# Performance work log

Hardware: AMD Instinct MI355X
Metric: run time of the kernel (lower is better)

The kernel has to match this reference:

```python
import jax, jax.numpy as jnp
import numpy as np

B, T, E = 8, 2048, 512   # batch, tokens, embedding_dim
K, C = 8192, 8           # num_embeddings, codebook_dim
LN_EPS = 1e-5


def _layer_norm(x, g, b):
    mu = jnp.mean(x, axis=-1, keepdims=True)
    var = jnp.var(x, axis=-1, keepdims=True)
    return (x - mu) * jax.lax.rsqrt(var + LN_EPS) * g + b


def setup_inputs() -> dict:
    key = jax.random.key(0)
    ks = jax.random.split(key, 8)
    s_e = 1.0 / np.sqrt(E)
    s_c = 1.0 / np.sqrt(C)
    return {
        "features": jax.random.normal(ks[0], (B, T, E), dtype=jnp.float32),
        # project_in: Linear(E,E) -> ReLU -> Linear(E,C)
        "W1_in": jax.random.uniform(ks[1], (E, E), jnp.float32, -s_e, s_e),
        "b1_in": jnp.zeros((E,), jnp.float32),
        "W2_in": jax.random.uniform(ks[2], (E, C), jnp.float32, -s_e, s_e),
        "b2_in": jnp.zeros((C,), jnp.float32),
        "ln_in_g": jnp.ones((C,), jnp.float32),
        "ln_in_b": jnp.zeros((C,), jnp.float32),
        # codebook
        "emb": jax.random.normal(ks[3], (K, C), dtype=jnp.float32),
        # project_out: Linear(C,E) -> ReLU -> Linear(E,E)
        "W1_out": jax.random.uniform(ks[4], (C, E), jnp.float32, -s_c, s_c),
        "b1_out": jnp.zeros((E,), jnp.float32),
        "W2_out": jax.random.uniform(ks[5], (E, E), jnp.float32, -s_e, s_e),
        "b2_out": jnp.zeros((E,), jnp.float32),
        "ln_out_g": jnp.ones((E,), jnp.float32),
        "ln_out_b": jnp.zeros((E,), jnp.float32),
    }


def reference(features, W1_in, b1_in, W2_in, b2_in, ln_in_g, ln_in_b, emb,
              W1_out, b1_out, W2_out, b2_out, ln_out_g, ln_out_b):
    # project_in + norm_in
    h = jax.nn.relu(jnp.einsum('bte,ef->btf', features, W1_in) + b1_in)
    z = jnp.einsum('bte,ec->btc', h, W2_in) + b2_in          # (B,T,C)
    z = _layer_norm(z, ln_in_g, ln_in_b)
    zf = z.reshape(-1, C)                                     # (N,C)
    d = (jnp.sum(zf * zf, axis=1, keepdims=True)
         - 2.0 * zf @ emb.T
         + jnp.sum(emb * emb, axis=1)[None, :])               # (N,K)
    idx = jnp.argmin(d, axis=1)                               # (N,)
    encodings = jax.nn.one_hot(idx, K, dtype=zf.dtype)        # (N,K)
    quantized = emb[idx]                                      # gather == one_hot @ emb
    # project_out + norm_out
    q = jax.nn.relu(quantized @ W1_out + b1_out)
    q = q @ W2_out + b2_out
    q = _layer_norm(q, ln_out_g, ln_out_b)
    q = q.reshape(B, T, E)
    return q, idx[:, None], encodings
```

## Files before the change

### kernel.cpp

```cpp
#include <hip/hip_runtime.h>
#include <cstdint>
#include <cstddef>

#define N_TOK 16384
#define E_DIM 512
#define C_DIM 8
#define K_CODES 8192
#define LN_EPS 1e-5f

typedef __attribute__((ext_vector_type(8))) short short8;
typedef __attribute__((ext_vector_type(4))) float f32x4;

__device__ __forceinline__ unsigned short bf16_rn(float x) {
  unsigned u = __float_as_uint(x);
  unsigned r = u + 0x7FFFu + ((u >> 16) & 1u);
  return (unsigned short)(r >> 16);
}
__device__ __forceinline__ float bf16_f(unsigned short h) {
  return __uint_as_float(((unsigned)h) << 16);
}

__device__ __forceinline__ void gload16(const void* g, void* l) {
  __builtin_amdgcn_global_load_lds(
      (const __attribute__((address_space(1))) void*)g,
      (__attribute__((address_space(3))) void*)l, 16, 0, 0);
}

__global__ __launch_bounds__(256) void pack_a(const float* __restrict__ A,
    unsigned short* __restrict__ hi, unsigned short* __restrict__ lo) {
  int t = blockIdx.x * 256 + threadIdx.x;
  int l = t & 63;
  int kt = (t >> 6) & 15;
  int mf = t >> 10;
  const float* src = A + (size_t)(mf * 16 + (l & 15)) * 512 + kt * 32 + (l >> 4) * 8;
  float4 x0 = *(const float4*)src;
  float4 x1 = *(const float4*)(src + 4);
  float xs[8] = {x0.x, x0.y, x0.z, x0.w, x1.x, x1.y, x1.z, x1.w};
  unsigned hw[4], lw[4];
#pragma unroll
  for (int p = 0; p < 4; ++p) {
    float a = xs[2 * p], b = xs[2 * p + 1];
    unsigned short ha = bf16_rn(a), hb = bf16_rn(b);
    unsigned short la = bf16_rn(a - bf16_f(ha)), lb = bf16_rn(b - bf16_f(hb));
    hw[p] = (unsigned)ha | ((unsigned)hb << 16);
    lw[p] = (unsigned)la | ((unsigned)lb << 16);
  }
  uint4 hv; hv.x = hw[0]; hv.y = hw[1]; hv.z = hw[2]; hv.w = hw[3];
  uint4 lv; lv.x = lw[0]; lv.y = lw[1]; lv.z = lw[2]; lv.w = lw[3];
  ((uint4*)hi)[t] = hv;
  ((uint4*)lo)[t] = lv;
}

__global__ __launch_bounds__(256) void pack_b(const float* __restrict__ B,
    unsigned short* __restrict__ hi, unsigned short* __restrict__ lo) {
  int t = blockIdx.x * 256 + threadIdx.x;
  int l = t & 63;
  int kt = (t >> 6) & 15;
  int nf = t >> 10;
  int col = nf * 16 + (l & 15);
  int krow = kt * 32 + (l >> 4) * 8;
  unsigned hw[4], lw[4];
#pragma unroll
  for (int p = 0; p < 4; ++p) {
    float a = B[(size_t)(krow + 2 * p) * 512 + col];
    float b = B[(size_t)(krow + 2 * p + 1) * 512 + col];
    unsigned short ha = bf16_rn(a), hb = bf16_rn(b);
    unsigned short la = bf16_rn(a - bf16_f(ha)), lb = bf16_rn(b - bf16_f(hb));
    hw[p] = (unsigned)ha | ((unsigned)hb << 16);
    lw[p] = (unsigned)la | ((unsigned)lb << 16);
  }
  uint4 hv; hv.x = hw[0]; hv.y = hw[1]; hv.z = hw[2]; hv.w = hw[3];
  uint4 lv; lv.x = lw[0]; lv.y = lw[1]; lv.z = lw[2]; lv.w = lw[3];
  ((uint4*)hi)[t] = hv;
  ((uint4*)lo)[t] = lv;
}

template<bool RELU>
__global__ __launch_bounds__(256) void gemm_mfma(const unsigned short* __restrict__ Ah,
    const unsigned short* __restrict__ Al, const unsigned short* __restrict__ Bh,
    const unsigned short* __restrict__ Bl, const float* __restrict__ bias,
    float* __restrict__ C) {
  __shared__ char smem[32768];
  const int tid = threadIdx.x;
  const int l = tid & 63;
  const int w = tid >> 6;
  const int wm = w >> 1, wn = w & 1;
  const int mblk = blockIdx.y, nblk = blockIdx.x;

  char* sAh = smem;
  char* sAl = smem + 8192;
  char* sBh = smem + 16384;
  char* sBl = smem + 24576;

  const char* gAh = (const char*)Ah + (((size_t)(mblk * 8 + 2 * w) * 16) * 64 + l) * 16;
  const char* gAl = (const char*)Al + (((size_t)(mblk * 8 + 2 * w) * 16) * 64 + l) * 16;
  const char* gBh = (const char*)Bh + (((size_t)(nblk * 8 + 2 * w) * 16) * 64 + l) * 16;
  const char* gBl = (const char*)Bl + (((size_t)(nblk * 8 + 2 * w) * 16) * 64 + l) * 16;
  char* dA0 = sAh + (2 * w) * 1024;
  char* dA1 = sAl + (2 * w) * 1024;
  char* dB0 = sBh + (2 * w) * 1024;
  char* dB1 = sBl + (2 * w) * 1024;

  f32x4 acc[4][4];
#pragma unroll
  for (int i = 0; i < 4; ++i)
#pragma unroll
    for (int j = 0; j < 4; ++j) acc[i][j] = (f32x4){0.f, 0.f, 0.f, 0.f};

  for (int kt = 0; kt < 16; ++kt) {
    __syncthreads();
    const size_t ko = (size_t)kt * 1024;
    gload16(gAh + ko,           dA0);
    gload16(gAh + ko + 16384,   dA0 + 1024);
    gload16(gAl + ko,           dA1);
    gload16(gAl + ko + 16384,   dA1 + 1024);
    gload16(gBh + ko,           dB0);
    gload16(gBh + ko + 16384,   dB0 + 1024);
    gload16(gBl + ko,           dB1);
    gload16(gBl + ko + 16384,   dB1 + 1024);
    __syncthreads();

    short8 a_h[4], a_l[4], b_h[4], b_l[4];
#pragma unroll
    for (int i = 0; i < 4; ++i) {
      a_h[i] = ((const short8*)sAh)[(wm * 4 + i) * 64 + l];
      a_l[i] = ((const short8*)sAl)[(wm * 4 + i) * 64 + l];
    }
#pragma unroll
    for (int j = 0; j < 4; ++j) {
      b_h[j] = ((const short8*)sBh)[(wn * 4 + j) * 64 + l];
      b_l[j] = ((const short8*)sBl)[(wn * 4 + j) * 64 + l];
    }
#pragma unroll
    for (int i = 0; i < 4; ++i)
#pragma unroll
      for (int j = 0; j < 4; ++j) {
        acc[i][j] = __builtin_amdgcn_mfma_f32_16x16x32_bf16(a_h[i], b_h[j], acc[i][j], 0, 0, 0);
        acc[i][j] = __builtin_amdgcn_mfma_f32_16x16x32_bf16(a_h[i], b_l[j], acc[i][j], 0, 0, 0);
        acc[i][j] = __builtin_amdgcn_mfma_f32_16x16x32_bf16(a_l[i], b_h[j], acc[i][j], 0, 0, 0);
      }
  }

  const int colb = nblk * 128 + wn * 64 + (l & 15);
  const int rowb = mblk * 128 + wm * 64 + ((l >> 4) << 2);
#pragma unroll
  for (int j = 0; j < 4; ++j) {
    float bv = bias[colb + j * 16];
#pragma unroll
    for (int i = 0; i < 4; ++i) {
#pragma unroll
      for (int r = 0; r < 4; ++r) {
        float v = acc[i][j][r] + bv;
        if (RELU) v = fmaxf(v, 0.f);
        C[(size_t)(rowb + i * 16 + r) * 512 + colb + j * 16] = v;
      }
    }
  }
}

__global__ __launch_bounds__(256) void zln_kernel(const float* __restrict__ h,
    const float* __restrict__ W2, const float* __restrict__ b2,
    const float* __restrict__ g, const float* __restrict__ b,
    float* __restrict__ z) {
  int token = blockIdx.x * 4 + (threadIdx.x >> 6);
  int lane = threadIdx.x & 63;
  const float* hr = h + (size_t)token * E_DIM;
  float acc[C_DIM];
#pragma unroll
  for (int c = 0; c < C_DIM; ++c) acc[c] = 0.f;
  for (int e = lane; e < E_DIM; e += 64) {
    float hv = hr[e];
    const float* w = W2 + e * C_DIM;
#pragma unroll
    for (int c = 0; c < C_DIM; ++c) acc[c] = fmaf(hv, w[c], acc[c]);
  }
#pragma unroll
  for (int c = 0; c < C_DIM; ++c) {
#pragma unroll
    for (int off = 32; off > 0; off >>= 1) acc[c] += __shfl_down(acc[c], off);
  }
  if (lane == 0) {
    float v[C_DIM]; float mu = 0.f;
#pragma unroll
    for (int c = 0; c < C_DIM; ++c) { v[c] = acc[c] + b2[c]; mu += v[c]; }
    mu *= 0.125f;
    float var = 0.f;
#pragma unroll
    for (int c = 0; c < C_DIM; ++c) { float d = v[c] - mu; var += d * d; }
    var *= 0.125f;
    float inv = 1.0f / sqrtf(var + LN_EPS);
#pragma unroll
    for (int c = 0; c < C_DIM; ++c)
      z[(size_t)token * C_DIM + c] = ((v[c] - mu) * inv) * g[c] + b[c];
  }
}

__global__ void ne_kernel(const float* __restrict__ emb, float* __restrict__ ne) {
  int k = blockIdx.x * 256 + threadIdx.x;
  const float* e = emb + (size_t)k * C_DIM;
  float s = 0.f;
#pragma unroll
  for (int c = 0; c < C_DIM; ++c) s = fmaf(e[c], e[c], s);
  ne[k] = s;
}

__global__ __launch_bounds__(256) void vq_partial(const float* __restrict__ z,
    const float* __restrict__ emb, const float* __restrict__ ne,
    float* __restrict__ pbest, int* __restrict__ pidx) {
  int chunk = blockIdx.x & 7;
  int token = (blockIdx.x >> 3) * 256 + threadIdx.x;
  float zv[C_DIM];
#pragma unroll
  for (int c = 0; c < C_DIM; ++c) zv[c] = z[(size_t)token * C_DIM + c];
  float s = 0.f;
#pragma unroll
  for (int c = 0; c < C_DIM; ++c) s = fmaf(zv[c], zv[c], s);
  float best = 3.402823466e38f; int bi = 0;
  int j0 = chunk * 1024;
  for (int j = j0; j < j0 + 1024; ++j) {
    const float* e = emb + (size_t)j * C_DIM;
    float p = 0.f;
#pragma unroll
    for (int c = 0; c < C_DIM; ++c) p = fmaf(zv[c], e[c], p);
    float d = fmaf(-2.f, p, s) + ne[j];
    if (d < best) { best = d; bi = j; }
  }
  pbest[chunk * N_TOK + token] = best;
  pidx[chunk * N_TOK + token] = bi;
}

__global__ void vq_combine(const float* __restrict__ pbest, const int* __restrict__ pidx,
    int* __restrict__ idx_i, float* __restrict__ idxf) {
  int n = blockIdx.x * 256 + threadIdx.x;
  float best = pbest[n]; int bi = pidx[n];
#pragma unroll
  for (int c = 1; c < 8; ++c) {
    float bb = pbest[c * N_TOK + n]; int i2 = pidx[c * N_TOK + n];
    if (bb < best) { best = bb; bi = i2; }
  }
  idx_i[n] = bi;
  idxf[n] = (float)bi;
}

__global__ __launch_bounds__(128) void proj_out1(const float* __restrict__ emb,
    const float* __restrict__ W1, const float* __restrict__ b1, float* __restrict__ t) {
  int k = blockIdx.x;
  int e = threadIdx.x * 4;
  float4 acc = *(const float4*)(b1 + e);
#pragma unroll
  for (int c = 0; c < C_DIM; ++c) {
    float ev = emb[(size_t)k * C_DIM + c];
    float4 w = *(const float4*)(W1 + (size_t)c * E_DIM + e);
    acc.x = fmaf(ev, w.x, acc.x); acc.y = fmaf(ev, w.y, acc.y);
    acc.z = fmaf(ev, w.z, acc.z); acc.w = fmaf(ev, w.w, acc.w);
  }
  acc.x = fmaxf(acc.x, 0.f); acc.y = fmaxf(acc.y, 0.f);
  acc.z = fmaxf(acc.z, 0.f); acc.w = fmaxf(acc.w, 0.f);
  *(float4*)(t + (size_t)k * E_DIM + e) = acc;
}

__global__ __launch_bounds__(256) void ln512(float* __restrict__ g,
    const float* __restrict__ gw, const float* __restrict__ bw) {
  int row = blockIdx.x; int tid = threadIdx.x;
  float* r = g + (size_t)row * E_DIM;
  float v0 = r[tid], v1 = r[tid + 256];
  __shared__ float red[8];
  int lane = tid & 63, wid = tid >> 6;
  float sum = v0 + v1;
#pragma unroll
  for (int off = 32; off > 0; off >>= 1) sum += __shfl_xor(sum, off);
  if (lane == 0) red[wid] = sum;
  __syncthreads();
  float mu = (red[0] + red[1] + red[2] + red[3]) * (1.0f / 512.0f);
  float d0 = v0 - mu, d1 = v1 - mu;
  float sq = d0 * d0 + d1 * d1;
#pragma unroll
  for (int off = 32; off > 0; off >>= 1) sq += __shfl_xor(sq, off);
  if (lane == 0) red[4 + wid] = sq;
  __syncthreads();
  float var = (red[4] + red[5] + red[6] + red[7]) * (1.0f / 512.0f);
  float inv = 1.0f / sqrtf(var + LN_EPS);
  r[tid]       = (d0 * inv) * gw[tid] + bw[tid];
  r[tid + 256] = (d1 * inv) * gw[tid + 256] + bw[tid + 256];
}

__global__ __launch_bounds__(128) void out_gather(const float* __restrict__ oc,
    const int* __restrict__ idx_i, float* __restrict__ q) {
  int n = blockIdx.x;
  int k = idx_i[n];
  int e = threadIdx.x * 4;
  *(float4*)(q + (size_t)n * E_DIM + e) = *(const float4*)(oc + (size_t)k * E_DIM + e);
}

__global__ void scatter_ones(const float* __restrict__ idxf, float* __restrict__ enc) {
  int n = blockIdx.x * 256 + threadIdx.x;
  int k = (int)idxf[n];
  enc[(size_t)n * K_CODES + k] = 1.0f;
}

extern "C" void kernel_launch(void* const* d_in, const int* in_sizes, int n_in,
                              void* d_out, int out_size, void* d_ws, size_t ws_size,
                              hipStream_t stream) {
  const float* features = (const float*)d_in[0];
  const float* W1_in  = (const float*)d_in[1];
  const float* b1_in  = (const float*)d_in[2];
  const float* W2_in  = (const float*)d_in[3];
  const float* b2_in  = (const float*)d_in[4];
  const float* ln_in_g = (const float*)d_in[5];
  const float* ln_in_b = (const float*)d_in[6];
  const float* emb    = (const float*)d_in[7];
  const float* W1_out = (const float*)d_in[8];
  const float* b1_out = (const float*)d_in[9];
  const float* W2_out = (const float*)d_in[10];
  const float* b2_out = (const float*)d_in[11];
  const float* ln_out_g = (const float*)d_in[12];
  const float* ln_out_b = (const float*)d_in[13];

  float* q    = (float*)d_out;
  float* idxf = q + (size_t)N_TOK * E_DIM;
  float* enc  = idxf + N_TOK;

  float* h     = enc;
  float* t     = enc + 8388608;
  float* g     = enc + 12582912;
  float* z     = enc + 16777216;
  float* ne    = enc + 16908288;
  float* pbest = enc + 16916480;
  int*   idx_i = (int*)(enc + 17047552);
  int*   pidx  = (int*)(enc + 17063936);
  unsigned short* A1h = (unsigned short*)(enc + 17195008);
  unsigned short* A1l = (unsigned short*)(enc + 21389312);
  unsigned short* A2h = (unsigned short*)(enc + 25583616);
  unsigned short* A2l = (unsigned short*)(enc + 27680768);
  unsigned short* B1h = (unsigned short*)(enc + 29777920);
  unsigned short* B1l = (unsigned short*)(enc + 29908992);
  unsigned short* B2h = (unsigned short*)(enc + 30040064);
  unsigned short* B2l = (unsigned short*)(enc + 30171136);

  ne_kernel<<<K_CODES / 256, 256, 0, stream>>>(emb, ne);

  pack_b<<<128, 256, 0, stream>>>(W1_in, B1h, B1l);
  pack_a<<<4096, 256, 0, stream>>>(features, A1h, A1l);
  dim3 g1(4, N_TOK / 128);
  gemm_mfma<true><<<g1, 256, 0, stream>>>(A1h, A1l, B1h, B1l, b1_in, h);

  zln_kernel<<<N_TOK / 4, 256, 0, stream>>>(h, W2_in, b2_in, ln_in_g, ln_in_b, z);

  vq_partial<<<(N_TOK / 256) * 8, 256, 0, stream>>>(z, emb, ne, pbest, pidx);
  vq_combine<<<N_TOK / 256, 256, 0, stream>>>(pbest, pidx, idx_i, idxf);

  proj_out1<<<K_CODES, 128, 0, stream>>>(emb, W1_out, b1_out, t);
  pack_b<<<128, 256, 0, stream>>>(W2_out, B2h, B2l);
  pack_a<<<2048, 256, 0, stream>>>(t, A2h, A2l);
  dim3 g2(4, K_CODES / 128);
  gemm_mfma<false><<<g2, 256, 0, stream>>>(A2h, A2l, B2h, B2l, b2_out, g);

  ln512<<<K_CODES, 256, 0, stream>>>(g, ln_out_g, ln_out_b);

  out_gather<<<N_TOK, 128, 0, stream>>>(g, idx_i, q);

  hipMemsetAsync(enc, 0, (size_t)N_TOK * K_CODES * sizeof(float), stream);
  scatter_ones<<<N_TOK / 256, 256, 0, stream>>>(idxf, enc);
}
```

Measured before the change: 793.8 us.

## Fuse pack kernels into prep, double-buffer GEMM LDS, fuse proj_out1 with packing

Merges the ne, pack_a and both pack_b launches into a single prep kernel. It also fuses the first output projection with bf16 hi/lo packing, so the float intermediate t is never written or re-read. The MFMA GEMM now double-buffers LDS stages so the next k-tile's global-to-LDS loads are issued while the current tile computes. LDS use doubles to 64KB per block, which may lower occupancy.

```diff
diff --git a/kernel.cpp b/kernel.cpp
--- a/kernel.cpp
+++ b/kernel.cpp
@@ -26,9 +26,8 @@
       (__attribute__((address_space(3))) void*)l, 16, 0, 0);
 }
 
-__global__ __launch_bounds__(256) void pack_a(const float* __restrict__ A,
-    unsigned short* __restrict__ hi, unsigned short* __restrict__ lo) {
-  int t = blockIdx.x * 256 + threadIdx.x;
+__device__ __forceinline__ void pack_a_body(const float* __restrict__ A,
+    unsigned short* __restrict__ hi, unsigned short* __restrict__ lo, int t) {
   int l = t & 63;
   int kt = (t >> 6) & 15;
   int mf = t >> 10;
@@ -51,9 +50,8 @@
   ((uint4*)lo)[t] = lv;
 }
 
-__global__ __launch_bounds__(256) void pack_b(const float* __restrict__ B,
-    unsigned short* __restrict__ hi, unsigned short* __restrict__ lo) {
-  int t = blockIdx.x * 256 + threadIdx.x;
+__device__ __forceinline__ void pack_b_body(const float* __restrict__ B,
+    unsigned short* __restrict__ hi, unsigned short* __restrict__ lo, int t) {
   int l = t & 63;
   int kt = (t >> 6) & 15;
   int nf = t >> 10;
@@ -75,31 +73,47 @@
   ((uint4*)lo)[t] = lv;
 }
 
+__global__ __launch_bounds__(256) void prep(const float* __restrict__ features,
+    const float* __restrict__ W1_in, const float* __restrict__ W2_out,
+    const float* __restrict__ emb,
+    unsigned short* __restrict__ A1h, unsigned short* __restrict__ A1l,
+    unsigned short* __restrict__ B1h, unsigned short* __restrict__ B1l,
+    unsigned short* __restrict__ B2h, unsigned short* __restrict__ B2l,
+    float* __restrict__ ne) {
+  int bid = blockIdx.x;
+  int tid = threadIdx.x;
+  if (bid < 4096) {
+    pack_a_body(features, A1h, A1l, bid * 256 + tid);
+  } else if (bid < 4224) {
+    pack_b_body(W1_in, B1h, B1l, (bid - 4096) * 256 + tid);
+  } else if (bid < 4352) {
+    pack_b_body(W2_out, B2h, B2l, (bid - 4224) * 256 + tid);
+  } else {
+    int k = (bid - 4352) * 256 + tid;
+    const float* e = emb + (size_t)k * C_DIM;
+    float s = 0.f;
+#pragma unroll
+    for (int c = 0; c < C_DIM; ++c) s = fmaf(e[c], e[c], s);
+    ne[k] = s;
+  }
+}
+
 template<bool RELU>
 __global__ __launch_bounds__(256) void gemm_mfma(const unsigned short* __restrict__ Ah,
     const unsigned short* __restrict__ Al, const unsigned short* __restrict__ Bh,
     const unsigned short* __restrict__ Bl, const float* __restrict__ bias,
     float* __restrict__ C) {
-  __shared__ char smem[32768];
+  __shared__ char smem[65536];
   const int tid = threadIdx.x;
   const int l = tid & 63;
   const int w = tid >> 6;
   const int wm = w >> 1, wn = w & 1;
   const int mblk = blockIdx.y, nblk = blockIdx.x;
 
-  char* sAh = smem;
-  char* sAl = smem + 8192;
-  char* sBh = smem + 16384;
-  char* sBl = smem + 24576;
-
   const char* gAh = (const char*)Ah + (((size_t)(mblk * 8 + 2 * w) * 16) * 64 + l) * 16;
   const char* gAl = (const char*)Al + (((size_t)(mblk * 8 + 2 * w) * 16) * 64 + l) * 16;
   const char* gBh = (const char*)Bh + (((size_t)(nblk * 8 + 2 * w) * 16) * 64 + l) * 16;
   const char* gBl = (const char*)Bl + (((size_t)(nblk * 8 + 2 * w) * 16) * 64 + l) * 16;
-  char* dA0 = sAh + (2 * w) * 1024;
-  char* dA1 = sAl + (2 * w) * 1024;
-  char* dB0 = sBh + (2 * w) * 1024;
-  char* dB1 = sBl + (2 * w) * 1024;
 
   f32x4 acc[4][4];
 #pragma unroll
@@ -107,29 +121,39 @@
 #pragma unroll
     for (int j = 0; j < 4; ++j) acc[i][j] = (f32x4){0.f, 0.f, 0.f, 0.f};
 
-  for (int kt = 0; kt < 16; ++kt) {
-    __syncthreads();
+  auto stage = [&](int buf, int kt) {
+    char* base = smem + buf * 32768;
     const size_t ko = (size_t)kt * 1024;
-    gload16(gAh + ko,           dA0);
-    gload16(gAh + ko + 16384,   dA0 + 1024);
-    gload16(gAl + ko,           dA1);
-    gload16(gAl + ko + 16384,   dA1 + 1024);
-    gload16(gBh + ko,           dB0);
-    gload16(gBh + ko + 16384,   dB0 + 1024);
-    gload16(gBl + ko,           dB1);
-    gload16(gBl + ko + 16384,   dB1 + 1024);
-    __syncthreads();
-
+    char* dA0 = base + (2 * w) * 1024;
+    char* dA1 = base + 8192 + (2 * w) * 1024;
+    char* dB0 = base + 16384 + (2 * w) * 1024;
+    char* dB1 = base + 24576 + (2 * w) * 1024;
+    gload16(gAh + ko,         dA0);
+    gload16(gAh + ko + 16384, dA0 + 1024);
+    gload16(gAl + ko,         dA1);
+    gload16(gAl + ko + 16384, dA1 + 1024);
+    gload16(gBh + ko,         dB0);
+    gload16(gBh + ko + 16384, dB0 + 1024);
+    gload16(gBl + ko,         dB1);
+    gload16(gBl + ko + 16384, dB1 + 1024);
+  };
+
+  auto compute = [&](int buf) {
+    const char* base = smem + buf * 32768;
+    const short8* sAh = (const short8*)(base);
+    const short8* sAl = (const short8*)(base + 8192);
+    const short8* sBh = (const short8*)(base + 16384);
+    const short8* sBl = (const short8*)(base + 24576);
     short8 a_h[4], a_l[4], b_h[4], b_l[4];
 #pragma unroll
     for (int i = 0; i < 4; ++i) {
-      a_h[i] = ((const short8*)sAh)[(wm * 4 + i) * 64 + l];
-      a_l[i] = ((const short8*)sAl)[(wm * 4 + i) * 64 + l];
+      a_h[i] = sAh[(wm * 4 + i) * 64 + l];
+      a_l[i] = sAl[(wm * 4 + i) * 64 + l];
     }
 #pragma unroll
     for (int j = 0; j < 4; ++j) {
-      b_h[j] = ((const short8*)sBh)[(wn * 4 + j) * 64 + l];
-      b_l[j] = ((const short8*)sBl)[(wn * 4 + j) * 64 + l];
+      b_h[j] = sBh[(wn * 4 + j) * 64 + l];
+      b_l[j] = sBl[(wn * 4 + j) * 64 + l];
     }
 #pragma unroll
     for (int i = 0; i < 4; ++i)
@@ -139,7 +163,19 @@
         acc[i][j] = __builtin_amdgcn_mfma_f32_16x16x32_bf16(a_h[i], b_l[j], acc[i][j], 0, 0, 0);
         acc[i][j] = __builtin_amdgcn_mfma_f32_16x16x32_bf16(a_l[i], b_h[j], acc[i][j], 0, 0, 0);
       }
-  }
+  };
+
+  stage(0, 0);
+  __syncthreads();
+  int cur = 0;
+#pragma unroll 1
+  for (int kt = 1; kt < 16; ++kt) {
+    stage(cur ^ 1, kt);
+    compute(cur);
+    __syncthreads();
+    cur ^= 1;
+  }
+  compute(cur);
 
   const int colb = nblk * 128 + wn * 64 + (l & 15);
   const int rowb = mblk * 128 + wm * 64 + ((l >> 4) << 2);
@@ -195,15 +231,6 @@
   }
 }
 
-__global__ void ne_kernel(const float* __restrict__ emb, float* __restrict__ ne) {
-  int k = blockIdx.x * 256 + threadIdx.x;
-  const float* e = emb + (size_t)k * C_DIM;
-  float s = 0.f;
-#pragma unroll
-  for (int c = 0; c < C_DIM; ++c) s = fmaf(e[c], e[c], s);
-  ne[k] = s;
-}
-
 __global__ __launch_bounds__(256) void vq_partial(const float* __restrict__ z,
     const float* __restrict__ emb, const float* __restrict__ ne,
     float* __restrict__ pbest, int* __restrict__ pidx) {
@@ -242,21 +269,49 @@
   idxf[n] = (float)bi;
 }
 
-__global__ __launch_bounds__(128) void proj_out1(const float* __restrict__ emb,
-    const float* __restrict__ W1, const float* __restrict__ b1, float* __restrict__ t) {
-  int k = blockIdx.x;
-  int e = threadIdx.x * 4;
-  float4 acc = *(const float4*)(b1 + e);
-#pragma unroll
-  for (int c = 0; c < C_DIM; ++c) {
-    float ev = emb[(size_t)k * C_DIM + c];
-    float4 w = *(const float4*)(W1 + (size_t)c * E_DIM + e);
-    acc.x = fmaf(ev, w.x, acc.x); acc.y = fmaf(ev, w.y, acc.y);
-    acc.z = fmaf(ev, w.z, acc.z); acc.w = fmaf(ev, w.w, acc.w);
-  }
-  acc.x = fmaxf(acc.x, 0.f); acc.y = fmaxf(acc.y, 0.f);
-  acc.z = fmaxf(acc.z, 0.f); acc.w = fmaxf(acc.w, 0.f);
-  *(float4*)(t + (size_t)k * E_DIM + e) = acc;
+__global__ __launch_bounds__(256) void proj_out1_pack(const float* __restrict__ emb,
+    const float* __restrict__ W1, const float* __restrict__ b1,
+    unsigned short* __restrict__ hi, unsigned short* __restrict__ lo) {
+  int mf = blockIdx.x;
+  int l = threadIdx.x & 63;
+  int kt4 = threadIdx.x >> 6;
+  int k0 = mf * 16 + (l & 15);
+  float ev[C_DIM];
+#pragma unroll
+  for (int c = 0; c < C_DIM; ++c) ev[c] = emb[(size_t)k0 * C_DIM + c];
+#pragma unroll
+  for (int it = 0; it < 4; ++it) {
+    int kt = it * 4 + kt4;
+    int e0 = kt * 32 + (l >> 4) * 8;
+    float o[8];
+    float4 bv0 = *(const float4*)(b1 + e0);
+    float4 bv1 = *(const float4*)(b1 + e0 + 4);
+    o[0] = bv0.x; o[1] = bv0.y; o[2] = bv0.z; o[3] = bv0.w;
+    o[4] = bv1.x; o[5] = bv1.y; o[6] = bv1.z; o[7] = bv1.w;
+#pragma unroll
+    for (int c = 0; c < C_DIM; ++c) {
+      float4 w0 = *(const float4*)(W1 + (size_t)c * E_DIM + e0);
+      float4 w1 = *(const float4*)(W1 + (size_t)c * E_DIM + e0 + 4);
+      o[0] = fmaf(ev[c], w0.x, o[0]); o[1] = fmaf(ev[c], w0.y, o[1]);
+      o[2] = fmaf(ev[c], w0.z, o[2]); o[3] = fmaf(ev[c], w0.w, o[3]);
+      o[4] = fmaf(ev[c], w1.x, o[4]); o[5] = fmaf(ev[c], w1.y, o[5]);
+      o[6] = fmaf(ev[c], w1.z, o[6]); o[7] = fmaf(ev[c], w1.w, o[7]);
+    }
+    unsigned hw[4], lw[4];
+#pragma unroll
+    for (int p = 0; p < 4; ++p) {
+      float a = fmaxf(o[2 * p], 0.f), b = fmaxf(o[2 * p + 1], 0.f);
+      unsigned short ha = bf16_rn(a), hb = bf16_rn(b);
+      unsigned short la = bf16_rn(a - bf16_f(ha)), lb = bf16_rn(b - bf16_f(hb));
+      hw[p] = (unsigned)ha | ((unsigned)hb << 16);
+      lw[p] = (unsigned)la | ((unsigned)lb << 16);
+    }
+    size_t t = ((size_t)mf * 16 + kt) * 64 + l;
+    uint4 hv; hv.x = hw[0]; hv.y = hw[1]; hv.z = hw[2]; hv.w = hw[3];
+    uint4 lv; lv.x = lw[0]; lv.y = lw[1]; lv.z = lw[2]; lv.w = lw[3];
+    ((uint4*)hi)[t] = hv;
+    ((uint4*)lo)[t] = lv;
+  }
 }
 
 __global__ __launch_bounds__(256) void ln512(float* __restrict__ g,
@@ -321,7 +376,6 @@
   float* enc  = idxf + N_TOK;
 
   float* h     = enc;
-  float* t     = enc + 8388608;
   float* g     = enc + 12582912;
   float* z     = enc + 16777216;
   float* ne    = enc + 16908288;
@@ -337,10 +391,9 @@
   unsigned short* B2h = (unsigned short*)(enc + 30040064);
   unsigned short* B2l = (unsigned short*)(enc + 30171136);
 
-  ne_kernel<<<K_CODES / 256, 256, 0, stream>>>(emb, ne);
-
-  pack_b<<<128, 256, 0, stream>>>(W1_in, B1h, B1l);
-  pack_a<<<4096, 256, 0, stream>>>(features, A1h, A1l);
+  prep<<<4384, 256, 0, stream>>>(features, W1_in, W2_out, emb,
+                                 A1h, A1l, B1h, B1l, B2h, B2l, ne);
+
   dim3 g1(4, N_TOK / 128);
   gemm_mfma<true><<<g1, 256, 0, stream>>>(A1h, A1l, B1h, B1l, b1_in, h);
 
@@ -349,9 +402,7 @@
   vq_partial<<<(N_TOK / 256) * 8, 256, 0, stream>>>(z, emb, ne, pbest, pidx);
   vq_combine<<<N_TOK / 256, 256, 0, stream>>>(pbest, pidx, idx_i, idxf);
 
-  proj_out1<<<K_CODES, 128, 0, stream>>>(emb, W1_out, b1_out, t);
-  pack_b<<<128, 256, 0, stream>>>(W2_out, B2h, B2l);
-  pack_a<<<2048, 256, 0, stream>>>(t, A2h, A2l);
+  proj_out1_pack<<<K_CODES / 16, 256, 0, stream>>>(emb, W1_out, b1_out, A2h, A2l);
   dim3 g2(4, K_CODES / 128);
   gemm_mfma<false><<<g2, 256, 0, stream>>>(A2h, A2l, B2h, B2l, b2_out, g);
 
```

After: 788.3 us. Within noise of the previous version (-0.7%).
